# Performance work log

Measured on AMD Instinct MI355X. Metric: run time of the kernel, lower is better.

## Reference

```python
import jax, jax.numpy as jnp
import numpy as np


def setup_inputs() -> dict:
    key = jax.random.key(0)
    k1, k2 = jax.random.split(key)
    B, Tq, Ts, H = 16, 2048, 2048, 1024
    hidden = jax.random.normal(k1, (B, Tq, H), dtype=jnp.float32)
    encoder_outputs = jax.random.normal(k2, (B, Ts, H), dtype=jnp.float32)
    return {"hidden": hidden, "encoder_outputs": encoder_outputs}


def reference(hidden, encoder_outputs):
    # scores[b, s, q] = <encoder_outputs[b, s], hidden[b, q]>  (no scaling)
    scores = jnp.einsum("bsh,bqh->bsq", encoder_outputs, hidden)
    # softmax over the source dimension s (dim=1, the NON-last axis)
    attn_weights = jax.nn.softmax(scores, axis=1)
    # context[b, q, h] = sum_s attn[b, s, q] * enc[b, s, h]
    context = jnp.einsum("bsq,bsh->bqh", attn_weights, encoder_outputs)
    return context
```

## Files before the change

kernel.cpp:

```cpp
#include <hip/hip_runtime.h>

#define NB_ 16
#define TQ_ 2048
#define TS_ 2048
#define DH_ 1024
#define QB_ 32
#define SB_ 256
#define NT_ 512

typedef _Float16 f16x8 __attribute__((ext_vector_type(8)));
typedef _Float16 f16x4 __attribute__((ext_vector_type(4)));
typedef float f32x4 __attribute__((ext_vector_type(4)));

__device__ inline uint32_t pack_h2(float a, float b) {
  union { _Float16 h[2]; uint32_t u; } c;
  c.h[0] = (_Float16)a; c.h[1] = (_Float16)b;
  return c.u;
}

__global__ void convert_f32_f16(const float* __restrict__ src, _Float16* __restrict__ dst) {
  size_t i = ((size_t)blockIdx.x * blockDim.x + threadIdx.x) * 8;
  float4 v0 = *(const float4*)(src + i);
  float4 v1 = *(const float4*)(src + i + 4);
  f16x8 o;
  o[0] = (_Float16)v0.x; o[1] = (_Float16)v0.y; o[2] = (_Float16)v0.z; o[3] = (_Float16)v0.w;
  o[4] = (_Float16)v1.x; o[5] = (_Float16)v1.y; o[6] = (_Float16)v1.z; o[7] = (_Float16)v1.w;
  *(f16x8*)(dst + i) = o;
}

__device__ inline f16x8 cvt8(const float* __restrict__ fp) {
  float4 a = *(const float4*)fp;
  float4 b = *(const float4*)(fp + 4);
  f16x8 t;
  t[0] = (_Float16)a.x; t[1] = (_Float16)a.y; t[2] = (_Float16)a.z; t[3] = (_Float16)a.w;
  t[4] = (_Float16)b.x; t[5] = (_Float16)b.y; t[6] = (_Float16)b.z; t[7] = (_Float16)b.w;
  return t;
}

template<bool WS16>
__device__ inline f16x8 ld8(const _Float16* __restrict__ hp, const float* __restrict__ fp, size_t idx) {
  if constexpr (WS16) return *(const f16x8*)(hp + idx);
  else return cvt8(fp + idx);
}

template<bool WS16>
__global__ __launch_bounds__(NT_, 2)
void attn_v12(const float* __restrict__ hid,
              const float* __restrict__ enc,
              const _Float16* __restrict__ encH,
              float* __restrict__ out) {
  __shared__ __attribute__((aligned(16))) char smem[148352];
  char*  const q_base = smem;
  float* const s_lds  = (float*)(smem + 65536);
  char*  const p_base = smem + 98816;
  char*  const vt_all = smem + 115200;
  float* const m_lds  = (float*)(smem + 147968);
  float* const l_lds  = m_lds + 32;
  float* const c_lds  = m_lds + 64;

  const int tid  = threadIdx.x;
  const int lane = tid & 63;
  const int wid  = tid >> 6;
  const int arow = lane & 15;
  const int agrp = lane >> 4;

  const int bi  = blockIdx.x;
  const int x   = bi & 7;
  const int idx = bi >> 3;
  const int b   = x + 8 * (idx >> 6);
  const int q0  = (idx & 63) * QB_;

  const int hw = wid;

  if (tid < 32) { m_lds[tid] = -__builtin_inff(); l_lds[tid] = 0.0f; }

  {
    const float* qsrc = hid + ((size_t)b * TQ_ + q0) * DH_;
    #pragma unroll
    for (int k = 0; k < 16; ++k) {
      int i = tid + k * NT_;
      int q = i >> 8;
      int h = (i & 255) * 4;
      float4 v = *(const float4*)(qsrc + (size_t)q * DH_ + h);
      int byte = (q * 2048 + h * 2) ^ ((q & 7) << 4);
      *(uint32_t*)(q_base + byte)     = pack_h2(v.x, v.y);
      *(uint32_t*)(q_base + byte + 4) = pack_h2(v.z, v.w);
    }
  }
  __syncthreads();

  f32x4 o_acc[2][8];
  #pragma unroll
  for (int m = 0; m < 2; ++m)
    #pragma unroll
    for (int n = 0; n < 8; ++n)
      o_acc[m][n] = {};

  char* const vt = vt_all + wid * 4096;
  const size_t enc_b = (size_t)b * TS_ * DH_;
  const int c8 = (lane & 7) * 8;
  const int d2 = (lane >> 3) * 2;

  for (int st = 0; st < TS_ / SB_; ++st) {
    const int s0 = st * SB_;

    f32x4 sacc[2][2] = {{{}, {}}, {{}, {}}};
    {
      const size_t krow = enc_b + (size_t)(s0 + wid * 32 + arow) * DH_;
      #pragma unroll
      for (int kf = 0; kf < 32; ++kf) {
        const int d = kf * 32 + agrp * 8;
        f16x8 bf0 = ld8<WS16>(encH, enc, krow + d);
        f16x8 bf1 = ld8<WS16>(encH, enc, krow + (size_t)16 * DH_ + d);
        f16x8 af0 = *(const f16x8*)(q_base + ((arow * 2048 + d * 2) ^ ((arow & 7) << 4)));
        f16x8 af1 = *(const f16x8*)(q_base + (((16 + arow) * 2048 + d * 2) ^ ((arow & 7) << 4)));
        sacc[0][0] = __builtin_amdgcn_mfma_f32_16x16x32_f16(af0, bf0, sacc[0][0], 0, 0, 0);
        sacc[0][1] = __builtin_amdgcn_mfma_f32_16x16x32_f16(af0, bf1, sacc[0][1], 0, 0, 0);
        sacc[1][0] = __builtin_amdgcn_mfma_f32_16x16x32_f16(af1, bf0, sacc[1][0], 0, 0, 0);
        sacc[1][1] = __builtin_amdgcn_mfma_f32_16x16x32_f16(af1, bf1, sacc[1][1], 0, 0, 0);
      }
    }

    f16x8 stgA[2][2], stgB[2][2];
    #pragma unroll
    for (int it = 0; it < 2; ++it) {
      size_t base = enc_b + (size_t)(s0 + it * 16 + d2) * DH_ + hw * 128 + c8;
      stgA[it][0] = ld8<WS16>(encH, enc, base);
      stgA[it][1] = ld8<WS16>(encH, enc, base + DH_);
    }

    {
      const int sc = wid * 32 + arow;
      #pragma unroll
      for (int m = 0; m < 2; ++m)
        #pragma unroll
        for (int n = 0; n < 2; ++n)
          #pragma unroll
          for (int i2 = 0; i2 < 4; ++i2)
            s_lds[(m * 16 + agrp * 4 + i2) * 260 + sc + n * 16] = sacc[m][n][i2];
    }

    __syncthreads();

    {
      int q = tid >> 4, sq = tid & 15;
      const float* bp = s_lds + q * 260 + sq * 16;
      f32x4 v0 = *(const f32x4*)bp;
      f32x4 v1 = *(const f32x4*)(bp + 4);
      f32x4 v2 = *(const f32x4*)(bp + 8);
      f32x4 v3 = *(const f32x4*)(bp + 12);
      f32x4 vm = v0;
      #pragma unroll
      for (int j = 0; j < 4; ++j) { vm[j] = fmaxf(fmaxf(v0[j], v1[j]), fmaxf(v2[j], v3[j])); }
      float mx = fmaxf(fmaxf(vm[0], vm[1]), fmaxf(vm[2], vm[3]));
      #pragma unroll
      for (int o = 8; o; o >>= 1) mx = fmaxf(mx, __shfl_xor(mx, o));
      float mprev = m_lds[q];
      float mnew  = fmaxf(mprev, mx);
      float p[16], ps = 0.0f;
      #pragma unroll
      for (int j = 0; j < 4; ++j) {
        p[j]      = __expf(v0[j] - mnew);
        p[4 + j]  = __expf(v1[j] - mnew);
        p[8 + j]  = __expf(v2[j] - mnew);
        p[12 + j] = __expf(v3[j] - mnew);
      }
      #pragma unroll
      for (int j = 0; j < 16; ++j) ps += p[j];
      #pragma unroll
      for (int o = 8; o; o >>= 1) ps += __shfl_xor(ps, o);
      if (sq == 0) {
        float cf = __expf(mprev - mnew);
        m_lds[q] = mnew;
        l_lds[q] = l_lds[q] * cf + ps;
        c_lds[q] = cf;
      }
      #pragma unroll
      for (int g = 0; g < 4; ++g) {
        f16x4 pw;
        pw[0] = (_Float16)p[g * 4 + 0]; pw[1] = (_Float16)p[g * 4 + 1];
        pw[2] = (_Float16)p[g * 4 + 2]; pw[3] = (_Float16)p[g * 4 + 3];
        *(f16x4*)(p_base + ((q * 512 + sq * 32 + g * 8) ^ ((q & 7) << 4))) = pw;
      }
    }

    __syncthreads();

    #pragma unroll
    for (int m = 0; m < 2; ++m)
      #pragma unroll
      for (int i2 = 0; i2 < 4; ++i2) {
        float cf = c_lds[m * 16 + agrp * 4 + i2];
        #pragma unroll
        for (int n = 0; n < 8; ++n) o_acc[m][n][i2] *= cf;
      }

    #pragma unroll
    for (int pass = 0; pass < 16; ++pass) {
      const int r  = pass >> 3, sp = pass & 7;
      const bool useA = (pass & 1) == 0;
      #pragma unroll
      for (int it = 0; it < 2; ++it) {
        int sl = it * 16 + d2;
        #pragma unroll
        for (int jj = 0; jj < 8; ++jj) {
          int hl = c8 + jj;
          union { _Float16 h[2]; uint32_t u; } pk;
          pk.h[0] = useA ? stgA[it][0][jj] : stgB[it][0][jj];
          pk.h[1] = useA ? stgA[it][1][jj] : stgB[it][1][jj];
          *(uint32_t*)(vt + ((hl * 64 + sl * 2) ^ (((hl >> 3) & 7) << 4))) = pk.u;
        }
      }
      if (pass < 15) {
        const int rn = (pass + 1) >> 3, spn = (pass + 1) & 7;
        #pragma unroll
        for (int it = 0; it < 2; ++it) {
          size_t base = enc_b + (size_t)(s0 + spn * 32 + it * 16 + d2) * DH_
                        + hw * 128 + rn * 64 + c8;
          if (useA) {
            stgB[it][0] = ld8<WS16>(encH, enc, base);
            stgB[it][1] = ld8<WS16>(encH, enc, base + DH_);
          } else {
            stgA[it][0] = ld8<WS16>(encH, enc, base);
            stgA[it][1] = ld8<WS16>(encH, enc, base + DH_);
          }
        }
      }
      f16x8 paf0 = *(const f16x8*)(p_base +
          ((arow * 512 + sp * 64 + agrp * 16) ^ ((arow & 7) << 4)));
      f16x8 paf1 = *(const f16x8*)(p_base +
          (((16 + arow) * 512 + sp * 64 + agrp * 16) ^ ((arow & 7) << 4)));
      __builtin_amdgcn_s_setprio(1);
      #pragma unroll
      for (int n = 0; n < 4; ++n) {
        int hl = n * 16 + arow;
        f16x8 bv = *(const f16x8*)(vt + ((hl * 64 + agrp * 16) ^ (((hl >> 3) & 7) << 4)));
        o_acc[0][r * 4 + n] = __builtin_amdgcn_mfma_f32_16x16x32_f16(paf0, bv, o_acc[0][r * 4 + n], 0, 0, 0);
        o_acc[1][r * 4 + n] = __builtin_amdgcn_mfma_f32_16x16x32_f16(paf1, bv, o_acc[1][r * 4 + n], 0, 0, 0);
      }
      __builtin_amdgcn_s_setprio(0);
    }
  }

  #pragma unroll
  for (int m = 0; m < 2; ++m) {
    #pragma unroll
    for (int i2 = 0; i2 < 4; ++i2) {
      int qr = m * 16 + agrp * 4 + i2;
      float inv = 1.0f / l_lds[qr];
      #pragma unroll
      for (int n = 0; n < 8; ++n) {
        out[((size_t)(b * TQ_ + q0 + qr)) * DH_ + hw * 128 + (n >> 2) * 64 + (n & 3) * 16 + arow] =
            o_acc[m][n][i2] * inv;
      }
    }
  }
}

extern "C" void kernel_launch(void* const* d_in, const int* in_sizes, int n_in,
                              void* d_out, int out_size, void* d_ws, size_t ws_size,
                              hipStream_t stream) {
  (void)in_sizes; (void)n_in; (void)out_size;
  const float* hid = (const float*)d_in[0];
  const float* enc = (const float*)d_in[1];
  float* out = (float*)d_out;

  const size_t encN = (size_t)NB_ * TS_ * DH_;
  const bool ws16 = (ws_size >= encN * sizeof(_Float16));

  dim3 grid(NB_ * (TQ_ / QB_), 1, 1);
  dim3 block(NT_, 1, 1);

  if (ws16) {
    _Float16* encH = (_Float16*)d_ws;
    convert_f32_f16<<<dim3((unsigned)(encN / 8 / 256)), dim3(256), 0, stream>>>(enc, encH);
    attn_v12<true><<<grid, block, 0, stream>>>(hid, enc, encH, out);
  } else {
    attn_v12<false><<<grid, block, 0, stream>>>(hid, enc, nullptr, out);
  }
}
```

Baseline: 741.9 us.

## Double S tile and do softmax in registers with cross-wave max/sum in LDS

Raises the source tile from 256 to 512 rows, so each wave computes a 32x64 score block. The scores are now computed transposed, which lets the softmax max and exp run directly on the MFMA accumulators using shuffles plus small per-wave partial max/sum arrays in LDS. This removes the full fp32 score staging buffer, halves the number of tile iterations, and uses lighter lgkmcnt-plus-barrier syncs with double-buffered running max/sum state. In exchange it adds more accumulator registers and longer PV loops per tile, which may hurt occupancy.

```diff
diff --git a/kernel.cpp b/kernel.cpp
--- a/kernel.cpp
+++ b/kernel.cpp
@@ -5,12 +5,15 @@
 #define TS_ 2048
 #define DH_ 1024
 #define QB_ 32
-#define SB_ 256
+#define SB_ 512
 #define NT_ 512
 
 typedef _Float16 f16x8 __attribute__((ext_vector_type(8)));
 typedef _Float16 f16x4 __attribute__((ext_vector_type(4)));
 typedef float f32x4 __attribute__((ext_vector_type(4)));
+typedef uint32_t u32x2 __attribute__((ext_vector_type(2)));
+
+#define LDS_BARRIER() asm volatile("s_waitcnt lgkmcnt(0)\n\ts_barrier" ::: "memory")
 
 __device__ inline uint32_t pack_h2(float a, float b) {
   union { _Float16 h[2]; uint32_t u; } c;
@@ -28,35 +31,35 @@
   *(f16x8*)(dst + i) = o;
 }
 
-__device__ inline f16x8 cvt8(const float* __restrict__ fp) {
-  float4 a = *(const float4*)fp;
-  float4 b = *(const float4*)(fp + 4);
-  f16x8 t;
-  t[0] = (_Float16)a.x; t[1] = (_Float16)a.y; t[2] = (_Float16)a.z; t[3] = (_Float16)a.w;
-  t[4] = (_Float16)b.x; t[5] = (_Float16)b.y; t[6] = (_Float16)b.z; t[7] = (_Float16)b.w;
-  return t;
-}
-
 template<bool WS16>
 __device__ inline f16x8 ld8(const _Float16* __restrict__ hp, const float* __restrict__ fp, size_t idx) {
-  if constexpr (WS16) return *(const f16x8*)(hp + idx);
-  else return cvt8(fp + idx);
+  if constexpr (WS16) {
+    return *(const f16x8*)(hp + idx);
+  } else {
+    float4 a = *(const float4*)(fp + idx);
+    float4 b = *(const float4*)(fp + idx + 4);
+    f16x8 t;
+    t[0] = (_Float16)a.x; t[1] = (_Float16)a.y; t[2] = (_Float16)a.z; t[3] = (_Float16)a.w;
+    t[4] = (_Float16)b.x; t[5] = (_Float16)b.y; t[6] = (_Float16)b.z; t[7] = (_Float16)b.w;
+    return t;
+  }
 }
 
 template<bool WS16>
 __global__ __launch_bounds__(NT_, 2)
-void attn_v12(const float* __restrict__ hid,
+void attn_v13(const float* __restrict__ hid,
               const float* __restrict__ enc,
               const _Float16* __restrict__ encH,
               float* __restrict__ out) {
-  __shared__ __attribute__((aligned(16))) char smem[148352];
+  __shared__ __attribute__((aligned(16))) char smem[133760];
   char*  const q_base = smem;
-  float* const s_lds  = (float*)(smem + 65536);
-  char*  const p_base = smem + 98816;
-  char*  const vt_all = smem + 115200;
-  float* const m_lds  = (float*)(smem + 147968);
-  float* const l_lds  = m_lds + 32;
-  float* const c_lds  = m_lds + 64;
+  char*  const p_lds  = smem + 65536;
+  char*  const vt_all = smem + 98304;
+  float* const pmax   = (float*)(smem + 131072);
+  float* const lsum   = (float*)(smem + 132096);
+  float* const mst    = (float*)(smem + 133120);
+  float* const lst    = (float*)(smem + 133376);
+  float* const c_lds  = (float*)(smem + 133632);
 
   const int tid  = threadIdx.x;
   const int lane = tid & 63;
@@ -72,7 +75,7 @@
 
   const int hw = wid;
 
-  if (tid < 32) { m_lds[tid] = -__builtin_inff(); l_lds[tid] = 0.0f; }
+  if (tid < 32) { mst[tid] = -__builtin_inff(); lst[tid] = 0.0f; }
 
   {
     const float* qsrc = hid + ((size_t)b * TQ_ + q0) * DH_;
@@ -103,21 +106,24 @@
 
   for (int st = 0; st < TS_ / SB_; ++st) {
     const int s0 = st * SB_;
-
-    f32x4 sacc[2][2] = {{{}, {}}, {{}, {}}};
+    const int p  = st & 1;
+
+    f32x4 sacc[4][2];
+    #pragma unroll
+    for (int t = 0; t < 4; ++t) { sacc[t][0] = {}; sacc[t][1] = {}; }
     {
-      const size_t krow = enc_b + (size_t)(s0 + wid * 32 + arow) * DH_;
+      const size_t krow = enc_b + (size_t)(s0 + wid * 64 + arow) * DH_;
       #pragma unroll
       for (int kf = 0; kf < 32; ++kf) {
         const int d = kf * 32 + agrp * 8;
-        f16x8 bf0 = ld8<WS16>(encH, enc, krow + d);
-        f16x8 bf1 = ld8<WS16>(encH, enc, krow + (size_t)16 * DH_ + d);
-        f16x8 af0 = *(const f16x8*)(q_base + ((arow * 2048 + d * 2) ^ ((arow & 7) << 4)));
-        f16x8 af1 = *(const f16x8*)(q_base + (((16 + arow) * 2048 + d * 2) ^ ((arow & 7) << 4)));
-        sacc[0][0] = __builtin_amdgcn_mfma_f32_16x16x32_f16(af0, bf0, sacc[0][0], 0, 0, 0);
-        sacc[0][1] = __builtin_amdgcn_mfma_f32_16x16x32_f16(af0, bf1, sacc[0][1], 0, 0, 0);
-        sacc[1][0] = __builtin_amdgcn_mfma_f32_16x16x32_f16(af1, bf0, sacc[1][0], 0, 0, 0);
-        sacc[1][1] = __builtin_amdgcn_mfma_f32_16x16x32_f16(af1, bf1, sacc[1][1], 0, 0, 0);
+        f16x8 qf0 = *(const f16x8*)(q_base + ((arow * 2048 + d * 2) ^ ((arow & 7) << 4)));
+        f16x8 qf1 = *(const f16x8*)(q_base + (((16 + arow) * 2048 + d * 2) ^ ((arow & 7) << 4)));
+        #pragma unroll
+        for (int t = 0; t < 4; ++t) {
+          f16x8 kfr = ld8<WS16>(encH, enc, krow + (size_t)(t * 16) * DH_ + d);
+          sacc[t][0] = __builtin_amdgcn_mfma_f32_16x16x32_f16(kfr, qf0, sacc[t][0], 0, 0, 0);
+          sacc[t][1] = __builtin_amdgcn_mfma_f32_16x16x32_f16(kfr, qf1, sacc[t][1], 0, 0, 0);
+        }
       }
     }
 
@@ -129,62 +135,74 @@
       stgA[it][1] = ld8<WS16>(encH, enc, base + DH_);
     }
 
-    {
-      const int sc = wid * 32 + arow;
-      #pragma unroll
-      for (int m = 0; m < 2; ++m)
-        #pragma unroll
-        for (int n = 0; n < 2; ++n)
-          #pragma unroll
-          for (int i2 = 0; i2 < 4; ++i2)
-            s_lds[(m * 16 + agrp * 4 + i2) * 260 + sc + n * 16] = sacc[m][n][i2];
-    }
-
-    __syncthreads();
-
-    {
-      int q = tid >> 4, sq = tid & 15;
-      const float* bp = s_lds + q * 260 + sq * 16;
-      f32x4 v0 = *(const f32x4*)bp;
-      f32x4 v1 = *(const f32x4*)(bp + 4);
-      f32x4 v2 = *(const f32x4*)(bp + 8);
-      f32x4 v3 = *(const f32x4*)(bp + 12);
-      f32x4 vm = v0;
-      #pragma unroll
-      for (int j = 0; j < 4; ++j) { vm[j] = fmaxf(fmaxf(v0[j], v1[j]), fmaxf(v2[j], v3[j])); }
-      float mx = fmaxf(fmaxf(vm[0], vm[1]), fmaxf(vm[2], vm[3]));
-      #pragma unroll
-      for (int o = 8; o; o >>= 1) mx = fmaxf(mx, __shfl_xor(mx, o));
-      float mprev = m_lds[q];
-      float mnew  = fmaxf(mprev, mx);
-      float p[16], ps = 0.0f;
-      #pragma unroll
-      for (int j = 0; j < 4; ++j) {
-        p[j]      = __expf(v0[j] - mnew);
-        p[4 + j]  = __expf(v1[j] - mnew);
-        p[8 + j]  = __expf(v2[j] - mnew);
-        p[12 + j] = __expf(v3[j] - mnew);
-      }
-      #pragma unroll
-      for (int j = 0; j < 16; ++j) ps += p[j];
-      #pragma unroll
-      for (int o = 8; o; o >>= 1) ps += __shfl_xor(ps, o);
-      if (sq == 0) {
-        float cf = __expf(mprev - mnew);
-        m_lds[q] = mnew;
-        l_lds[q] = l_lds[q] * cf + ps;
-        c_lds[q] = cf;
-      }
-      #pragma unroll
-      for (int g = 0; g < 4; ++g) {
-        f16x4 pw;
-        pw[0] = (_Float16)p[g * 4 + 0]; pw[1] = (_Float16)p[g * 4 + 1];
-        pw[2] = (_Float16)p[g * 4 + 2]; pw[3] = (_Float16)p[g * 4 + 3];
-        *(f16x4*)(p_base + ((q * 512 + sq * 32 + g * 8) ^ ((q & 7) << 4))) = pw;
-      }
-    }
-
-    __syncthreads();
+    float mprev[2], mnew[2];
+    #pragma unroll
+    for (int m = 0; m < 2; ++m) {
+      float pm = sacc[0][m][0];
+      #pragma unroll
+      for (int t = 0; t < 4; ++t)
+        #pragma unroll
+        for (int i2 = 0; i2 < 4; ++i2) pm = fmaxf(pm, sacc[t][m][i2]);
+      pm = fmaxf(pm, __shfl_xor(pm, 16));
+      pm = fmaxf(pm, __shfl_xor(pm, 32));
+      if (agrp == 0) pmax[wid * 32 + m * 16 + arow] = pm;
+    }
+
+    LDS_BARRIER();
+
+    #pragma unroll
+    for (int m = 0; m < 2; ++m) {
+      const int q = m * 16 + arow;
+      float mv = mst[p * 32 + q];
+      mprev[m] = mv;
+      #pragma unroll
+      for (int w = 0; w < 8; ++w) mv = fmaxf(mv, pmax[w * 32 + q]);
+      mnew[m] = mv;
+    }
+
+    #pragma unroll
+    for (int m = 0; m < 2; ++m) {
+      const int q = m * 16 + arow;
+      float ls = 0.0f;
+      #pragma unroll
+      for (int t = 0; t < 4; ++t) {
+        float e0 = __expf(sacc[t][m][0] - mnew[m]);
+        float e1 = __expf(sacc[t][m][1] - mnew[m]);
+        float e2 = __expf(sacc[t][m][2] - mnew[m]);
+        float e3 = __expf(sacc[t][m][3] - mnew[m]);
+        ls += (e0 + e1) + (e2 + e3);
+        u32x2 pw;
+        pw[0] = pack_h2(e0, e1);
+        pw[1] = pack_h2(e2, e3);
+        const int s_loc = wid * 64 + t * 16 + agrp * 4;
+        *(u32x2*)(p_lds + ((q * 1024 + s_loc * 2) ^ ((arow & 7) << 4))) = pw;
+      }
+      ls += __shfl_xor(ls, 16);
+      ls += __shfl_xor(ls, 32);
+      if (agrp == 0) lsum[wid * 32 + q] = ls;
+    }
+
+    if (wid == 0 && agrp == 0) {
+      #pragma unroll
+      for (int m = 0; m < 2; ++m) {
+        const int q = m * 16 + arow;
+        c_lds[q] = __expf(mprev[m] - mnew[m]);
+        mst[(p ^ 1) * 32 + q] = mnew[m];
+      }
+    }
+
+    LDS_BARRIER();
+
+    if (wid == 0 && agrp == 0) {
+      #pragma unroll
+      for (int m = 0; m < 2; ++m) {
+        const int q = m * 16 + arow;
+        float s8 = 0.0f;
+        #pragma unroll
+        for (int w = 0; w < 8; ++w) s8 += lsum[w * 32 + q];
+        lst[(p ^ 1) * 32 + q] = lst[p * 32 + q] * c_lds[q] + s8;
+      }
+    }
 
     #pragma unroll
     for (int m = 0; m < 2; ++m)
@@ -196,8 +214,8 @@
       }
 
     #pragma unroll
-    for (int pass = 0; pass < 16; ++pass) {
-      const int r  = pass >> 3, sp = pass & 7;
+    for (int pass = 0; pass < 32; ++pass) {
+      const int r  = pass >> 4, sp = pass & 15;
       const bool useA = (pass & 1) == 0;
       #pragma unroll
       for (int it = 0; it < 2; ++it) {
@@ -211,8 +229,8 @@
           *(uint32_t*)(vt + ((hl * 64 + sl * 2) ^ (((hl >> 3) & 7) << 4))) = pk.u;
         }
       }
-      if (pass < 15) {
-        const int rn = (pass + 1) >> 3, spn = (pass + 1) & 7;
+      if (pass < 31) {
+        const int rn = (pass + 1) >> 4, spn = (pass + 1) & 15;
         #pragma unroll
         for (int it = 0; it < 2; ++it) {
           size_t base = enc_b + (size_t)(s0 + spn * 32 + it * 16 + d2) * DH_
@@ -226,10 +244,10 @@
           }
         }
       }
-      f16x8 paf0 = *(const f16x8*)(p_base +
-          ((arow * 512 + sp * 64 + agrp * 16) ^ ((arow & 7) << 4)));
-      f16x8 paf1 = *(const f16x8*)(p_base +
-          (((16 + arow) * 512 + sp * 64 + agrp * 16) ^ ((arow & 7) << 4)));
+      f16x8 paf0 = *(const f16x8*)(p_lds +
+          ((arow * 1024 + sp * 64 + agrp * 16) ^ ((arow & 7) << 4)));
+      f16x8 paf1 = *(const f16x8*)(p_lds +
+          (((16 + arow) * 1024 + sp * 64 + agrp * 16) ^ ((arow & 7) << 4)));
       __builtin_amdgcn_s_setprio(1);
       #pragma unroll
       for (int n = 0; n < 4; ++n) {
@@ -242,12 +260,14 @@
     }
   }
 
+  LDS_BARRIER();
+
   #pragma unroll
   for (int m = 0; m < 2; ++m) {
     #pragma unroll
     for (int i2 = 0; i2 < 4; ++i2) {
       int qr = m * 16 + agrp * 4 + i2;
-      float inv = 1.0f / l_lds[qr];
+      float inv = 1.0f / lst[qr];
       #pragma unroll
       for (int n = 0; n < 8; ++n) {
         out[((size_t)(b * TQ_ + q0 + qr)) * DH_ + hw * 128 + (n >> 2) * 64 + (n & 3) * 16 + arow] =
@@ -274,8 +294,8 @@
   if (ws16) {
     _Float16* encH = (_Float16*)d_ws;
     convert_f32_f16<<<dim3((unsigned)(encN / 8 / 256)), dim3(256), 0, stream>>>(enc, encH);
-    attn_v12<true><<<grid, block, 0, stream>>>(hid, enc, encH, out);
+    attn_v13<true><<<grid, block, 0, stream>>>(hid, enc, encH, out);
   } else {
-    attn_v12<false><<<grid, block, 0, stream>>>(hid, enc, nullptr, out);
-  }
-}
+    attn_v13<false><<<grid, block, 0, stream>>>(hid, enc, nullptr, out);
+  }
+}
```

After: 912.7 us. +23.0%, slower.

## Pre-transpose encoder to f16 in workspace and read V directly from global

Applied to the files above, without the earlier changes.

The conversion kernel now writes a second, transposed f16 copy of the encoder outputs along with the row-major one. The PV stage loads its B operands straight from that transposed copy in global memory, which removes the per-pass register staging, the LDS transpose writes and the LDS V tile. This frees about 32 KB of shared memory per block and drops LDS traffic. In exchange it needs twice the workspace, the pre-pass writes more data, and V-operand loads now depend on L2/global latency with no software prefetch.

```diff
diff --git a/kernel.cpp b/kernel.cpp
--- a/kernel.cpp
+++ b/kernel.cpp
@@ -18,14 +18,36 @@
   return c.u;
 }
 
-__global__ void convert_f32_f16(const float* __restrict__ src, _Float16* __restrict__ dst) {
-  size_t i = ((size_t)blockIdx.x * blockDim.x + threadIdx.x) * 8;
-  float4 v0 = *(const float4*)(src + i);
-  float4 v1 = *(const float4*)(src + i + 4);
-  f16x8 o;
-  o[0] = (_Float16)v0.x; o[1] = (_Float16)v0.y; o[2] = (_Float16)v0.z; o[3] = (_Float16)v0.w;
-  o[4] = (_Float16)v1.x; o[5] = (_Float16)v1.y; o[6] = (_Float16)v1.z; o[7] = (_Float16)v1.w;
-  *(f16x8*)(dst + i) = o;
+__global__ void conv_tr(const float* __restrict__ src,
+                        _Float16* __restrict__ dH,
+                        _Float16* __restrict__ dT) {
+  const int b  = blockIdx.x;
+  const int st = blockIdx.y;
+  const int ht = blockIdx.z;
+  const int tid = threadIdx.x;
+  __shared__ _Float16 t[64][72];
+
+  const size_t base = ((size_t)b * TS_ + (size_t)st * 64) * DH_ + (size_t)ht * 64;
+  #pragma unroll
+  for (int k = 0; k < 16; ++k) {
+    int i = k * 256 + tid;
+    int sl = i >> 6, hl = i & 63;
+    float v = src[base + (size_t)sl * DH_ + hl];
+    _Float16 h = (_Float16)v;
+    dH[base + (size_t)sl * DH_ + hl] = h;
+    t[sl][hl] = h;
+  }
+  __syncthreads();
+  const size_t tbase = ((size_t)b * DH_ + (size_t)ht * 64) * TS_ + (size_t)st * 64;
+  #pragma unroll
+  for (int k = 0; k < 8; ++k) {
+    int i = k * 256 + tid;
+    int hl = i >> 5, s2 = (i & 31) * 2;
+    union { _Float16 h[2]; uint32_t u; } pk;
+    pk.h[0] = t[s2][hl];
+    pk.h[1] = t[s2 + 1][hl];
+    *(uint32_t*)((_Float16*)dT + tbase + (size_t)hl * TS_ + s2) = pk.u;
+  }
 }
 
 __device__ inline f16x8 cvt8(const float* __restrict__ fp) {
@@ -37,24 +59,18 @@
   return t;
 }
 
-template<bool WS16>
-__device__ inline f16x8 ld8(const _Float16* __restrict__ hp, const float* __restrict__ fp, size_t idx) {
-  if constexpr (WS16) return *(const f16x8*)(hp + idx);
-  else return cvt8(fp + idx);
-}
-
-template<bool WS16>
+template<int MODE>
 __global__ __launch_bounds__(NT_, 2)
-void attn_v12(const float* __restrict__ hid,
+void attn_v14(const float* __restrict__ hid,
               const float* __restrict__ enc,
               const _Float16* __restrict__ encH,
+              const _Float16* __restrict__ encT,
               float* __restrict__ out) {
-  __shared__ __attribute__((aligned(16))) char smem[148352];
+  __shared__ __attribute__((aligned(16))) char smem[115584];
   char*  const q_base = smem;
   float* const s_lds  = (float*)(smem + 65536);
   char*  const p_base = smem + 98816;
-  char*  const vt_all = smem + 115200;
-  float* const m_lds  = (float*)(smem + 147968);
+  float* const m_lds  = (float*)(smem + 115200);
   float* const l_lds  = m_lds + 32;
   float* const c_lds  = m_lds + 64;
 
@@ -96,10 +112,8 @@
     for (int n = 0; n < 8; ++n)
       o_acc[m][n] = {};
 
-  char* const vt = vt_all + wid * 4096;
-  const size_t enc_b = (size_t)b * TS_ * DH_;
-  const int c8 = (lane & 7) * 8;
-  const int d2 = (lane >> 3) * 2;
+  const size_t enc_b  = (size_t)b * TS_ * DH_;
+  const size_t encT_b = (size_t)b * DH_ * TS_;
 
   for (int st = 0; st < TS_ / SB_; ++st) {
     const int s0 = st * SB_;
@@ -110,8 +124,14 @@
       #pragma unroll
       for (int kf = 0; kf < 32; ++kf) {
         const int d = kf * 32 + agrp * 8;
-        f16x8 bf0 = ld8<WS16>(encH, enc, krow + d);
-        f16x8 bf1 = ld8<WS16>(encH, enc, krow + (size_t)16 * DH_ + d);
+        f16x8 bf0, bf1;
+        if constexpr (MODE == 1) {
+          bf0 = *(const f16x8*)(encH + krow + d);
+          bf1 = *(const f16x8*)(encH + krow + (size_t)16 * DH_ + d);
+        } else {
+          bf0 = cvt8(enc + krow + d);
+          bf1 = cvt8(enc + krow + (size_t)16 * DH_ + d);
+        }
         f16x8 af0 = *(const f16x8*)(q_base + ((arow * 2048 + d * 2) ^ ((arow & 7) << 4)));
         f16x8 af1 = *(const f16x8*)(q_base + (((16 + arow) * 2048 + d * 2) ^ ((arow & 7) << 4)));
         sacc[0][0] = __builtin_amdgcn_mfma_f32_16x16x32_f16(af0, bf0, sacc[0][0], 0, 0, 0);
@@ -119,14 +139,6 @@
         sacc[1][0] = __builtin_amdgcn_mfma_f32_16x16x32_f16(af1, bf0, sacc[1][0], 0, 0, 0);
         sacc[1][1] = __builtin_amdgcn_mfma_f32_16x16x32_f16(af1, bf1, sacc[1][1], 0, 0, 0);
       }
-    }
-
-    f16x8 stgA[2][2], stgB[2][2];
-    #pragma unroll
-    for (int it = 0; it < 2; ++it) {
-      size_t base = enc_b + (size_t)(s0 + it * 16 + d2) * DH_ + hw * 128 + c8;
-      stgA[it][0] = ld8<WS16>(encH, enc, base);
-      stgA[it][1] = ld8<WS16>(encH, enc, base + DH_);
     }
 
     {
@@ -196,47 +208,25 @@
       }
 
     #pragma unroll
-    for (int pass = 0; pass < 16; ++pass) {
-      const int r  = pass >> 3, sp = pass & 7;
-      const bool useA = (pass & 1) == 0;
-      #pragma unroll
-      for (int it = 0; it < 2; ++it) {
-        int sl = it * 16 + d2;
-        #pragma unroll
-        for (int jj = 0; jj < 8; ++jj) {
-          int hl = c8 + jj;
-          union { _Float16 h[2]; uint32_t u; } pk;
-          pk.h[0] = useA ? stgA[it][0][jj] : stgB[it][0][jj];
-          pk.h[1] = useA ? stgA[it][1][jj] : stgB[it][1][jj];
-          *(uint32_t*)(vt + ((hl * 64 + sl * 2) ^ (((hl >> 3) & 7) << 4))) = pk.u;
+    for (int ks = 0; ks < 8; ++ks) {
+      f16x8 paf0 = *(const f16x8*)(p_base +
+          ((arow * 512 + ks * 64 + agrp * 16) ^ ((arow & 7) << 4)));
+      f16x8 paf1 = *(const f16x8*)(p_base +
+          (((16 + arow) * 512 + ks * 64 + agrp * 16) ^ ((arow & 7) << 4)));
+      __builtin_amdgcn_s_setprio(1);
+      #pragma unroll
+      for (int n = 0; n < 8; ++n) {
+        const int hg = hw * 128 + n * 16 + arow;
+        f16x8 bv;
+        if constexpr (MODE == 1) {
+          bv = *(const f16x8*)(encT + encT_b + (size_t)hg * TS_ + s0 + ks * 32 + agrp * 8);
+        } else {
+          #pragma unroll
+          for (int j = 0; j < 8; ++j)
+            bv[j] = (_Float16)enc[enc_b + (size_t)(s0 + ks * 32 + agrp * 8 + j) * DH_ + hg];
         }
-      }
-      if (pass < 15) {
-        const int rn = (pass + 1) >> 3, spn = (pass + 1) & 7;
-        #pragma unroll
-        for (int it = 0; it < 2; ++it) {
-          size_t base = enc_b + (size_t)(s0 + spn * 32 + it * 16 + d2) * DH_
-                        + hw * 128 + rn * 64 + c8;
-          if (useA) {
-            stgB[it][0] = ld8<WS16>(encH, enc, base);
-            stgB[it][1] = ld8<WS16>(encH, enc, base + DH_);
-          } else {
-            stgA[it][0] = ld8<WS16>(encH, enc, base);
-            stgA[it][1] = ld8<WS16>(encH, enc, base + DH_);
-          }
-        }
-      }
-      f16x8 paf0 = *(const f16x8*)(p_base +
-          ((arow * 512 + sp * 64 + agrp * 16) ^ ((arow & 7) << 4)));
-      f16x8 paf1 = *(const f16x8*)(p_base +
-          (((16 + arow) * 512 + sp * 64 + agrp * 16) ^ ((arow & 7) << 4)));
-      __builtin_amdgcn_s_setprio(1);
-      #pragma unroll
-      for (int n = 0; n < 4; ++n) {
-        int hl = n * 16 + arow;
-        f16x8 bv = *(const f16x8*)(vt + ((hl * 64 + agrp * 16) ^ (((hl >> 3) & 7) << 4)));
-        o_acc[0][r * 4 + n] = __builtin_amdgcn_mfma_f32_16x16x32_f16(paf0, bv, o_acc[0][r * 4 + n], 0, 0, 0);
-        o_acc[1][r * 4 + n] = __builtin_amdgcn_mfma_f32_16x16x32_f16(paf1, bv, o_acc[1][r * 4 + n], 0, 0, 0);
+        o_acc[0][n] = __builtin_amdgcn_mfma_f32_16x16x32_f16(paf0, bv, o_acc[0][n], 0, 0, 0);
+        o_acc[1][n] = __builtin_amdgcn_mfma_f32_16x16x32_f16(paf1, bv, o_acc[1][n], 0, 0, 0);
       }
       __builtin_amdgcn_s_setprio(0);
     }
@@ -250,7 +240,7 @@
       float inv = 1.0f / l_lds[qr];
       #pragma unroll
       for (int n = 0; n < 8; ++n) {
-        out[((size_t)(b * TQ_ + q0 + qr)) * DH_ + hw * 128 + (n >> 2) * 64 + (n & 3) * 16 + arow] =
+        out[((size_t)(b * TQ_ + q0 + qr)) * DH_ + hw * 128 + n * 16 + arow] =
             o_acc[m][n][i2] * inv;
       }
     }
@@ -266,16 +256,18 @@
   float* out = (float*)d_out;
 
   const size_t encN = (size_t)NB_ * TS_ * DH_;
-  const bool ws16 = (ws_size >= encN * sizeof(_Float16));
+  const bool ws_ok = (ws_size >= 2 * encN * sizeof(_Float16));
 
   dim3 grid(NB_ * (TQ_ / QB_), 1, 1);
   dim3 block(NT_, 1, 1);
 
-  if (ws16) {
+  if (ws_ok) {
     _Float16* encH = (_Float16*)d_ws;
-    convert_f32_f16<<<dim3((unsigned)(encN / 8 / 256)), dim3(256), 0, stream>>>(enc, encH);
-    attn_v12<true><<<grid, block, 0, stream>>>(hid, enc, encH, out);
+    _Float16* encT = encH + encN;
+    dim3 cgrid(NB_, TS_ / 64, DH_ / 64);
+    conv_tr<<<cgrid, dim3(256), 0, stream>>>(enc, encH, encT);
+    attn_v14<1><<<grid, block, 0, stream>>>(hid, enc, encH, encT, out);
   } else {
-    attn_v12<false><<<grid, block, 0, stream>>>(hid, enc, nullptr, out);
-  }
-}
+    attn_v14<0><<<grid, block, 0, stream>>>(hid, enc, nullptr, nullptr, out);
+  }
+}
```

Result: slower. 1.217 ms (+64.1%).

## Prefetch V two passes ahead, widen transposed LDS stores, use lighter LDS barriers

Applied to the files above, without the earlier changes.

Each lane now loads 4 consecutive source rows of V per pass instead of two pairs, and writes the transposed V tile with 64-bit LDS stores. The loads are double-buffered two passes ahead rather than one, to hide more global latency. The two __syncthreads in the softmax phase are replaced by an inline-asm barrier that waits only on LDS counters, so in-flight global V prefetches are not forced to complete. This costs more live registers, which may pressure occupancy at 2 blocks per CU.

```diff
diff --git a/kernel.cpp b/kernel.cpp
--- a/kernel.cpp
+++ b/kernel.cpp
@@ -11,10 +11,18 @@
 typedef _Float16 f16x8 __attribute__((ext_vector_type(8)));
 typedef _Float16 f16x4 __attribute__((ext_vector_type(4)));
 typedef float f32x4 __attribute__((ext_vector_type(4)));
+typedef uint32_t u32x2 __attribute__((ext_vector_type(2)));
+
+#define LDS_BARRIER() asm volatile("s_waitcnt lgkmcnt(0)\n\ts_barrier" ::: "memory")
 
 __device__ inline uint32_t pack_h2(float a, float b) {
   union { _Float16 h[2]; uint32_t u; } c;
   c.h[0] = (_Float16)a; c.h[1] = (_Float16)b;
+  return c.u;
+}
+__device__ inline uint32_t pack_ff(_Float16 a, _Float16 b) {
+  union { _Float16 h[2]; uint32_t u; } c;
+  c.h[0] = a; c.h[1] = b;
   return c.u;
 }
 
@@ -45,7 +53,7 @@
 
 template<bool WS16>
 __global__ __launch_bounds__(NT_, 2)
-void attn_v12(const float* __restrict__ hid,
+void attn_v18(const float* __restrict__ hid,
               const float* __restrict__ enc,
               const _Float16* __restrict__ encH,
               float* __restrict__ out) {
@@ -98,11 +106,22 @@
 
   char* const vt = vt_all + wid * 4096;
   const size_t enc_b = (size_t)b * TS_ * DH_;
-  const int c8 = (lane & 7) * 8;
-  const int d2 = (lane >> 3) * 2;
+  const int h8 = (lane & 7) * 8;
+  const int s4 = (lane >> 3) * 4;
+
+  f16x8 stg[2][4];
 
   for (int st = 0; st < TS_ / SB_; ++st) {
     const int s0 = st * SB_;
+
+    auto loadV = [&](int pass, int slot) {
+      const int r = pass >> 3, sp = pass & 7;
+      size_t base = enc_b + (size_t)(s0 + sp * 32 + s4) * DH_ + hw * 128 + r * 64 + h8;
+      stg[slot][0] = ld8<WS16>(encH, enc, base);
+      stg[slot][1] = ld8<WS16>(encH, enc, base + DH_);
+      stg[slot][2] = ld8<WS16>(encH, enc, base + 2 * DH_);
+      stg[slot][3] = ld8<WS16>(encH, enc, base + 3 * DH_);
+    };
 
     f32x4 sacc[2][2] = {{{}, {}}, {{}, {}}};
     {
@@ -121,13 +140,8 @@
       }
     }
 
-    f16x8 stgA[2][2], stgB[2][2];
-    #pragma unroll
-    for (int it = 0; it < 2; ++it) {
-      size_t base = enc_b + (size_t)(s0 + it * 16 + d2) * DH_ + hw * 128 + c8;
-      stgA[it][0] = ld8<WS16>(encH, enc, base);
-      stgA[it][1] = ld8<WS16>(encH, enc, base + DH_);
-    }
+    loadV(0, 0);
+    loadV(1, 1);
 
     {
       const int sc = wid * 32 + arow;
@@ -140,7 +154,7 @@
             s_lds[(m * 16 + agrp * 4 + i2) * 260 + sc + n * 16] = sacc[m][n][i2];
     }
 
-    __syncthreads();
+    LDS_BARRIER();
 
     {
       int q = tid >> 4, sq = tid & 15;
@@ -184,7 +198,7 @@
       }
     }
 
-    __syncthreads();
+    LDS_BARRIER();
 
     #pragma unroll
     for (int m = 0; m < 2; ++m)
@@ -197,35 +211,17 @@
 
     #pragma unroll
     for (int pass = 0; pass < 16; ++pass) {
-      const int r  = pass >> 3, sp = pass & 7;
-      const bool useA = (pass & 1) == 0;
-      #pragma unroll
-      for (int it = 0; it < 2; ++it) {
-        int sl = it * 16 + d2;
-        #pragma unroll
-        for (int jj = 0; jj < 8; ++jj) {
-          int hl = c8 + jj;
-          union { _Float16 h[2]; uint32_t u; } pk;
-          pk.h[0] = useA ? stgA[it][0][jj] : stgB[it][0][jj];
-          pk.h[1] = useA ? stgA[it][1][jj] : stgB[it][1][jj];
-          *(uint32_t*)(vt + ((hl * 64 + sl * 2) ^ (((hl >> 3) & 7) << 4))) = pk.u;
-        }
-      }
-      if (pass < 15) {
-        const int rn = (pass + 1) >> 3, spn = (pass + 1) & 7;
-        #pragma unroll
-        for (int it = 0; it < 2; ++it) {
-          size_t base = enc_b + (size_t)(s0 + spn * 32 + it * 16 + d2) * DH_
-                        + hw * 128 + rn * 64 + c8;
-          if (useA) {
-            stgB[it][0] = ld8<WS16>(encH, enc, base);
-            stgB[it][1] = ld8<WS16>(encH, enc, base + DH_);
-          } else {
-            stgA[it][0] = ld8<WS16>(encH, enc, base);
-            stgA[it][1] = ld8<WS16>(encH, enc, base + DH_);
-          }
-        }
-      }
+      const int r    = pass >> 3, sp = pass & 7;
+      const int slot = pass & 1;
+      #pragma unroll
+      for (int jj = 0; jj < 8; ++jj) {
+        const int hl = h8 + jj;
+        u32x2 w;
+        w[0] = pack_ff(stg[slot][0][jj], stg[slot][1][jj]);
+        w[1] = pack_ff(stg[slot][2][jj], stg[slot][3][jj]);
+        *(u32x2*)(vt + ((hl * 64 + s4 * 2) ^ (((hl >> 3) & 7) << 4))) = w;
+      }
+      if (pass < 14) loadV(pass + 2, slot);
       f16x8 paf0 = *(const f16x8*)(p_base +
           ((arow * 512 + sp * 64 + agrp * 16) ^ ((arow & 7) << 4)));
       f16x8 paf1 = *(const f16x8*)(p_base +
@@ -233,7 +229,7 @@
       __builtin_amdgcn_s_setprio(1);
       #pragma unroll
       for (int n = 0; n < 4; ++n) {
-        int hl = n * 16 + arow;
+        const int hl = n * 16 + arow;
         f16x8 bv = *(const f16x8*)(vt + ((hl * 64 + agrp * 16) ^ (((hl >> 3) & 7) << 4)));
         o_acc[0][r * 4 + n] = __builtin_amdgcn_mfma_f32_16x16x32_f16(paf0, bv, o_acc[0][r * 4 + n], 0, 0, 0);
         o_acc[1][r * 4 + n] = __builtin_amdgcn_mfma_f32_16x16x32_f16(paf1, bv, o_acc[1][r * 4 + n], 0, 0, 0);
@@ -274,8 +270,8 @@
   if (ws16) {
     _Float16* encH = (_Float16*)d_ws;
     convert_f32_f16<<<dim3((unsigned)(encN / 8 / 256)), dim3(256), 0, stream>>>(enc, encH);
-    attn_v12<true><<<grid, block, 0, stream>>>(hid, enc, encH, out);
+    attn_v18<true><<<grid, block, 0, stream>>>(hid, enc, encH, out);
   } else {
-    attn_v12<false><<<grid, block, 0, stream>>>(hid, enc, nullptr, out);
-  }
-}
+    attn_v18<false><<<grid, block, 0, stream>>>(hid, enc, nullptr, out);
+  }
+}
```

After: 731.9 us. No clear change (-1.3%).
